# Kernel optimization log

Hardware: AMD Instinct MI355X
Metric: run time of the kernel (lower is better)

The kernel has to match this reference:

```python
import jax, jax.numpy as jnp
import numpy as np

N = 50000      # nodes
E = 800000     # edges
F = 128        # num_node_features
H = 128        # hidden_dim
DEPTH = 4
G = 512        # number of graphs in batch
BN_EPS = 1e-5


def setup_inputs() -> dict:
    key = jax.random.key(0)
    ks = jax.random.split(key, 10)
    x = jax.random.normal(ks[0], (N, F), dtype=jnp.float32)
    edge_index = jax.random.randint(ks[1], (2, E), 0, N, dtype=jnp.int64)
    batch = jnp.sort(jax.random.randint(ks[2], (N,), 0, G, dtype=jnp.int64))
    W_emb = jax.random.normal(ks[3], (F, H), dtype=jnp.float32) / np.sqrt(F)
    b_emb = jnp.zeros((H,), dtype=jnp.float32)
    W_conv = jax.random.normal(ks[4], (DEPTH, H, H), dtype=jnp.float32) / np.sqrt(H)
    b_conv = jnp.zeros((DEPTH, H), dtype=jnp.float32)
    gamma = jnp.ones((DEPTH - 1, H), dtype=jnp.float32)
    beta = jnp.zeros((DEPTH - 1, H), dtype=jnp.float32)
    return {"x": x, "edge_index": edge_index, "batch": batch,
            "W_emb": W_emb, "b_emb": b_emb, "W_conv": W_conv,
            "b_conv": b_conv, "gamma": gamma, "beta": beta}


def _gcn_conv(h, W, b, src, dst, dinv):
    # PyG GCNConv: D^{-1/2}(A+I)D^{-1/2} (h W) + b, with self-loops folded in
    hw = h @ W  # [N, H]
    norm = dinv[src] * dinv[dst]  # [E]
    agg = jax.ops.segment_sum(norm[:, None] * hw[src], dst, num_segments=N)
    agg = agg + (dinv * dinv)[:, None] * hw  # self-loop contribution
    return agg + b


def _batchnorm(h, g, b):
    mu = jnp.mean(h, axis=0)
    var = jnp.var(h, axis=0)
    return (h - mu) * jax.lax.rsqrt(var + BN_EPS) * g + b


def reference(x, edge_index, batch, W_emb, b_emb, W_conv, b_conv, gamma, beta):
    src, dst = edge_index[0], edge_index[1]
    # degrees incl. self-loop for symmetric GCN normalization
    deg = jax.ops.segment_sum(jnp.ones((E,), jnp.float32), dst, num_segments=N) + 1.0
    dinv = jax.lax.rsqrt(deg)
    h = x @ W_emb + b_emb  # embedding Linear
    for i in range(DEPTH):
        h = _gcn_conv(h, W_conv[i], b_conv[i], src, dst, dinv)
        if i < DEPTH - 1:
            h = jax.nn.relu(h)
            h = _batchnorm(h, gamma[i], beta[i])
    # global mean pool over graph ids
    counts = jax.ops.segment_sum(jnp.ones((N,), jnp.float32), batch, num_segments=G)
    pooled = jax.ops.segment_sum(h, batch, num_segments=G)
    return pooled / jnp.maximum(counts, 1.0)[:, None]
```

## Files before the change

kernel.cpp:

```cpp
#include <hip/hip_runtime.h>
#include <hip/hip_fp16.h>
#include <math.h>

#define HDIM 128
#define BKT_SHIFT 7
#define NBMAX 512
#define CHUNK 4096

typedef __attribute__((ext_vector_type(8))) short bf16x8;
typedef __attribute__((ext_vector_type(4))) float f32x4;

union U4 { unsigned int u[4]; bf16x8 v; };

__device__ __forceinline__ unsigned int cvt_pk_bf16(float a, float b) {
    unsigned int r;
    asm("v_cvt_pk_bf16_f32 %0, %1, %2" : "=v"(r) : "v"(a), "v"(b));
    return r;
}

__device__ __forceinline__ void split8(const float* v, bf16x8& ah, bf16x8& al) {
    U4 H, L;
    #pragma unroll
    for (int p = 0; p < 4; p++) {
        unsigned int h = cvt_pk_bf16(v[2 * p], v[2 * p + 1]);
        H.u[p] = h;
        float h0 = __uint_as_float(h << 16);
        float h1 = __uint_as_float(h & 0xFFFF0000u);
        L.u[p] = cvt_pk_bf16(v[2 * p] - h0, v[2 * p + 1] - h1);
    }
    ah = H.v; al = L.v;
}

__global__ __launch_bounds__(256) void bucket_hist(const int* __restrict__ dst,
                                                   int* __restrict__ bcount, int E) {
    __shared__ int h[NBMAX];
    int t = threadIdx.x;
    for (int b = t; b < NBMAX; b += 256) h[b] = 0;
    __syncthreads();
    int i = blockIdx.x * blockDim.x + t;
    int stride = gridDim.x * blockDim.x;
    for (; i < E; i += stride) atomicAdd(&h[dst[i] >> BKT_SHIFT], 1);
    __syncthreads();
    for (int b = t; b < NBMAX; b += 256) {
        int c = h[b];
        if (c) atomicAdd(&bcount[b], c);
    }
}

__global__ __launch_bounds__(256) void bucket_scan(const int* __restrict__ bcount,
                                                   int* __restrict__ bases,
                                                   int* __restrict__ cursor, int E) {
    int t = threadIdx.x;
    int v0 = bcount[2 * t], v1 = bcount[2 * t + 1];
    int s = v0 + v1;
    __shared__ int ss[256];
    ss[t] = s; __syncthreads();
    #pragma unroll
    for (int off = 1; off < 256; off <<= 1) {
        int u = (t >= off) ? ss[t - off] : 0;
        __syncthreads();
        ss[t] += u;
        __syncthreads();
    }
    int ex = ss[t] - s;
    bases[2 * t] = ex;          cursor[2 * t] = ex;
    bases[2 * t + 1] = ex + v0; cursor[2 * t + 1] = ex + v0;
    if (t == 255) bases[NBMAX] = E;
}

__global__ __launch_bounds__(256) void bucket_scatter(const int* __restrict__ src,
                                                      const int* __restrict__ dst,
                                                      int* __restrict__ cursor,
                                                      unsigned* __restrict__ ebuf, int E) {
    __shared__ unsigned sbuf[CHUNK];
    __shared__ int hist[NBMAX], hbase[NBMAX], gbase[NBMAX], cnt2[NBMAX];
    __shared__ int ss[256];
    int t = threadIdx.x;
    int start = blockIdx.x * CHUNK;
    int n = min(CHUNK, E - start);

    for (int b = t; b < NBMAX; b += 256) { hist[b] = 0; cnt2[b] = 0; }
    __syncthreads();
    for (int i = t; i < n; i += 256) atomicAdd(&hist[dst[start + i] >> BKT_SHIFT], 1);
    __syncthreads();

    int v0 = hist[2 * t], v1 = hist[2 * t + 1];
    int s = v0 + v1;
    ss[t] = s; __syncthreads();
    #pragma unroll
    for (int off = 1; off < 256; off <<= 1) {
        int u = (t >= off) ? ss[t - off] : 0;
        __syncthreads();
        ss[t] += u;
        __syncthreads();
    }
    int ex = ss[t] - s;
    hbase[2 * t] = ex;
    hbase[2 * t + 1] = ex + v0;
    if (v0 > 0) gbase[2 * t] = atomicAdd(&cursor[2 * t], v0);
    if (v1 > 0) gbase[2 * t + 1] = atomicAdd(&cursor[2 * t + 1], v1);
    __syncthreads();

    for (int i = t; i < n; i += 256) {
        int d = dst[start + i];
        int bkt = d >> BKT_SHIFT;
        unsigned p = ((unsigned)(d & 127) << 24) | (unsigned)src[start + i];
        int pos = atomicAdd(&cnt2[bkt], 1);
        sbuf[hbase[bkt] + pos] = p;
    }
    __syncthreads();

    for (int b = t; b < NBMAX; b += 256) {
        int c = hist[b], hb = hbase[b], gb = gbase[b];
        for (int j = 0; j < c; j++) ebuf[gb + j] = sbuf[hb + j];
    }
}

__global__ __launch_bounds__(256) void bucket_finalize(const unsigned* __restrict__ ebuf,
                                                       const int* __restrict__ bases,
                                                       int* __restrict__ csr,
                                                       int* __restrict__ offs,
                                                       float* __restrict__ dinv,
                                                       int N, int E) {
    int b = blockIdx.x;
    int beg = bases[b], end = bases[b + 1];
    __shared__ int hist[128], pre[128], cnt2[128];
    int t = threadIdx.x;
    if (t < 128) { hist[t] = 0; cnt2[t] = 0; }
    __syncthreads();
    for (int i = beg + t; i < end; i += 256)
        atomicAdd(&hist[(ebuf[i] >> 24) & 127], 1);
    __syncthreads();
    if (t < 128) pre[t] = hist[t];
    __syncthreads();
    #pragma unroll
    for (int off = 1; off < 128; off <<= 1) {
        int v = (t < 128 && t >= off) ? pre[t - off] : 0;
        __syncthreads();
        if (t < 128) pre[t] += v;
        __syncthreads();
    }
    if (t < 128) {
        int node = b * 128 + t;
        if (node < N) {
            int ex = pre[t] - hist[t];
            offs[node] = beg + ex;
            dinv[node] = rsqrtf((float)hist[t] + 1.0f);
        }
    }
    if (b == 0 && t == 0) offs[N] = E;
    __syncthreads();
    for (int i = beg + t; i < end; i += 256) {
        unsigned p = ebuf[i];
        int dl = (p >> 24) & 127;
        int pos = atomicAdd(&cnt2[dl], 1);
        csr[beg + (pre[dl] - hist[dl]) + pos] = (int)(p & 0xFFFFFFu);
    }
}

__global__ void wsplit_kernel(const float* __restrict__ Wsrc, short* __restrict__ Whi,
                              short* __restrict__ Wlo) {
    int i = blockIdx.x * 256 + threadIdx.x;
    if (i >= 128 * 128) return;
    int n = i >> 7, k = i & 127;
    float v = Wsrc[k * 128 + n];
    unsigned int u = __float_as_uint(v);
    unsigned int hi = (u + 0x7FFFu + ((u >> 16) & 1)) & 0xFFFF0000u;
    float hf = __uint_as_float(hi);
    float lo = v - hf;
    unsigned int ul = __float_as_uint(lo);
    unsigned int lo16 = (ul + 0x7FFFu + ((ul >> 16) & 1)) >> 16;
    Whi[i] = (short)(hi >> 16);
    Wlo[i] = (short)lo16;
}

template <bool OUT_F16>
__global__ __launch_bounds__(256) void gemm_mfma(const float* __restrict__ A,
                                                 const short* __restrict__ Wh,
                                                 const short* __restrict__ Wl,
                                                 const float* __restrict__ aff_s,
                                                 const float* __restrict__ aff_t,
                                                 const float* __restrict__ bias,
                                                 const float* __restrict__ rowscale,
                                                 void* __restrict__ outp, int N) {
    int w = threadIdx.x >> 6;
    int lane = threadIdx.x & 63;
    int l15 = lane & 15, lg = lane >> 4;
    int r0 = blockIdx.x * 128 + (w >> 1) * 64;
    int c0 = (w & 1) * 64;

    f32x4 acc[4][4];
    #pragma unroll
    for (int tc = 0; tc < 4; tc++) {
        float bz = bias ? bias[c0 + tc * 16 + l15] : 0.0f;
        #pragma unroll
        for (int tr = 0; tr < 4; tr++) {
            acc[tr][tc][0] = bz; acc[tr][tc][1] = bz;
            acc[tr][tc][2] = bz; acc[tr][tc][3] = bz;
        }
    }

    #pragma unroll
    for (int kt = 0; kt < 4; kt++) {
        int kk = kt * 32 + lg * 8;

        bf16x8 bh[4], bl[4];
        #pragma unroll
        for (int tc = 0; tc < 4; tc++) {
            int n = c0 + tc * 16 + l15;
            bh[tc] = *(const bf16x8*)(Wh + n * 128 + kk);
            bl[tc] = *(const bf16x8*)(Wl + n * 128 + kk);
        }

        float sv[8], tv[8];
        if (aff_s) {
            *(float4*)&sv[0] = *(const float4*)(aff_s + kk);
            *(float4*)&sv[4] = *(const float4*)(aff_s + kk + 4);
            *(float4*)&tv[0] = *(const float4*)(aff_t + kk);
            *(float4*)&tv[4] = *(const float4*)(aff_t + kk + 4);
        }

        bf16x8 ah[4], al[4];
        #pragma unroll
        for (int tr = 0; tr < 4; tr++) {
            int row = min(r0 + tr * 16 + l15, N - 1);
            const float* ap = A + (size_t)row * 128 + kk;
            float v[8];
            *(float4*)&v[0] = *(const float4*)ap;
            *(float4*)&v[4] = *(const float4*)(ap + 4);
            if (aff_s) {
                #pragma unroll
                for (int j = 0; j < 8; j++) v[j] = fmaf(v[j], sv[j], tv[j]);
            }
            split8(v, ah[tr], al[tr]);
        }

        #pragma unroll
        for (int tr = 0; tr < 4; tr++) {
            #pragma unroll
            for (int tc = 0; tc < 4; tc++) {
                acc[tr][tc] = __builtin_amdgcn_mfma_f32_16x16x32_bf16(ah[tr], bh[tc], acc[tr][tc], 0, 0, 0);
                acc[tr][tc] = __builtin_amdgcn_mfma_f32_16x16x32_bf16(ah[tr], bl[tc], acc[tr][tc], 0, 0, 0);
                acc[tr][tc] = __builtin_amdgcn_mfma_f32_16x16x32_bf16(al[tr], bh[tc], acc[tr][tc], 0, 0, 0);
            }
        }
    }

    #pragma unroll
    for (int tr = 0; tr < 4; tr++) {
        #pragma unroll
        for (int r = 0; r < 4; r++) {
            int row = r0 + tr * 16 + lg * 4 + r;
            if (row < N) {
                float sc = rowscale ? rowscale[row] : 1.0f;
                #pragma unroll
                for (int tc = 0; tc < 4; tc++) {
                    int col = c0 + tc * 16 + l15;
                    float val = acc[tr][tc][r] * sc;
                    if (OUT_F16) {
                        ((__half*)outp)[(size_t)row * 128 + col] = __float2half(val);
                    } else {
                        ((float*)outp)[(size_t)row * 128 + col] = val;
                    }
                }
            }
        }
    }
}

__global__ __launch_bounds__(256) void gather_kernel(const __half* __restrict__ hws,
                                                     const int* __restrict__ csr_src,
                                                     const int* __restrict__ offs,
                                                     const float* __restrict__ dinv,
                                                     const float* __restrict__ bias,
                                                     float* __restrict__ out,
                                                     int N, int relu) {
    int lane = threadIdx.x & 63;
    int node = blockIdx.x * 4 + (threadIdx.x >> 6);
    if (node >= N) return;
    int lo = offs[node], hi = offs[node + 1];

    float2 acc = make_float2(0.f, 0.f);
    int j = lo;
    for (; j + 3 < hi; j += 4) {
        int s0 = csr_src[j], s1 = csr_src[j + 1], s2 = csr_src[j + 2], s3 = csr_src[j + 3];
        float2 v0 = __half22float2(((const __half2*)(hws + (size_t)s0 * HDIM))[lane]);
        float2 v1 = __half22float2(((const __half2*)(hws + (size_t)s1 * HDIM))[lane]);
        float2 v2 = __half22float2(((const __half2*)(hws + (size_t)s2 * HDIM))[lane]);
        float2 v3 = __half22float2(((const __half2*)(hws + (size_t)s3 * HDIM))[lane]);
        acc.x += v0.x + v1.x + v2.x + v3.x;
        acc.y += v0.y + v1.y + v2.y + v3.y;
    }
    for (; j < hi; j++) {
        int s = csr_src[j];
        float2 v = __half22float2(((const __half2*)(hws + (size_t)s * HDIM))[lane]);
        acc.x += v.x; acc.y += v.y;
    }
    float2 vs = __half22float2(((const __half2*)(hws + (size_t)node * HDIM))[lane]);
    float di = dinv[node];
    float2 b = ((const float2*)bias)[lane];
    float ox = di * (acc.x + vs.x) + b.x;
    float oy = di * (acc.y + vs.y) + b.y;
    if (relu) { ox = fmaxf(ox, 0.f); oy = fmaxf(oy, 0.f); }
    ((float2*)(out + (size_t)node * HDIM))[lane] = make_float2(ox, oy);
}

__global__ __launch_bounds__(256) void bn_stats_kernel(const float* __restrict__ h,
                                                       float* __restrict__ stats, int N) {
    int f = threadIdx.x & 127;
    int half_ = threadIdx.x >> 7;
    float s = 0.f, s2 = 0.f;
    for (int n = blockIdx.x * 2 + half_; n < N; n += gridDim.x * 2) {
        float v = h[(size_t)n * HDIM + f];
        s += v;
        s2 += v * v;
    }
    __shared__ float ls[256], ls2[256];
    ls[threadIdx.x] = s;
    ls2[threadIdx.x] = s2;
    __syncthreads();
    if (half_ == 0) {
        s = ls[f] + ls[f + 128];
        s2 = ls2[f] + ls2[f + 128];
        atomicAdd(&stats[f], s);
        atomicAdd(&stats[128 + f], s2);
    }
}

__global__ void bn_finalize(const float* __restrict__ stats, const float* __restrict__ gamma,
                            const float* __restrict__ beta, float* __restrict__ aff_s,
                            float* __restrict__ aff_t, int N) {
    int f = threadIdx.x;
    float inv = 1.0f / (float)N;
    float m = stats[f] * inv;
    float var = stats[128 + f] * inv - m * m;
    float s = gamma[f] * rsqrtf(var + 1e-5f);
    aff_s[f] = s;
    aff_t[f] = beta[f] - m * s;
}

__device__ __forceinline__ int lower_bound_i(const int* __restrict__ arr, int n, int val) {
    int lo = 0, hi = n;
    while (lo < hi) {
        int mid = (lo + hi) >> 1;
        if (arr[mid] < val) lo = mid + 1; else hi = mid;
    }
    return lo;
}

__global__ void pool_kernel(const float* __restrict__ h, const int* __restrict__ batch,
                            float* __restrict__ out, int N, int G) {
    int g = blockIdx.x;
    int lo = lower_bound_i(batch, N, g);
    int hi = lower_bound_i(batch, N, g + 1);
    int f = threadIdx.x;
    float s = 0.f;
    for (int n = lo; n < hi; n++) s += h[(size_t)n * HDIM + f];
    float cnt = (float)(hi - lo);
    out[(size_t)g * HDIM + f] = s / fmaxf(cnt, 1.0f);
}

extern "C" void kernel_launch(void* const* d_in, const int* in_sizes, int n_in,
                              void* d_out, int out_size, void* d_ws, size_t ws_size,
                              hipStream_t stream) {
    const float* x      = (const float*)d_in[0];
    const int*   ei     = (const int*)d_in[1];
    const int*   batch  = (const int*)d_in[2];
    const float* W_emb  = (const float*)d_in[3];
    const float* b_emb  = (const float*)d_in[4];
    const float* W_conv = (const float*)d_in[5];
    const float* b_conv = (const float*)d_in[6];
    const float* gamma  = (const float*)d_in[7];
    const float* beta   = (const float*)d_in[8];

    const int E = in_sizes[1] / 2;
    const int N = in_sizes[2];
    const int G = out_size / HDIM;
    const int DEPTH = 4;

    const int* srcp = ei;
    const int* dstp = ei + E;
    float* out = (float*)d_out;

    size_t NH = (size_t)N * HDIM;
    size_t npad = ((size_t)N + 63) & ~(size_t)63;
    size_t epad = ((size_t)E + 63) & ~(size_t)63;
    int nb = (N + 127) / 128;

    float* ws = (float*)d_ws;
    float* dinv    = ws;
    int*   offs    = (int*)(dinv + npad);
    int*   bases   = offs + npad + 64;
    int*   cursor  = bases + 1024;
    int*   bcount  = cursor + NBMAX;
    int*   csr     = bcount + NBMAX;
    unsigned* ebuf = (unsigned*)(csr + epad);
    float* stats   = (float*)(ebuf + epad);
    float* aff_s   = stats + 256;
    float* aff_t   = aff_s + 128;
    short* wt      = (short*)(aff_t + 128);
    float* hbuf    = (float*)(wt + 5 * 2 * 16384);
    __half* hws16  = (__half*)(hbuf + NH);

    wsplit_kernel<<<64, 256, 0, stream>>>(W_emb, wt, wt + 16384);
    for (int l = 0; l < DEPTH; l++) {
        short* whi = wt + (size_t)(l + 1) * 32768;
        wsplit_kernel<<<64, 256, 0, stream>>>(W_conv + (size_t)l * 16384, whi, whi + 16384);
    }

    hipMemsetAsync(bcount, 0, NBMAX * sizeof(int), stream);
    bucket_hist<<<256, 256, 0, stream>>>(dstp, bcount, E);
    bucket_scan<<<1, 256, 0, stream>>>(bcount, bases, cursor, E);
    bucket_scatter<<<(E + CHUNK - 1) / CHUNK, 256, 0, stream>>>(srcp, dstp, cursor, ebuf, E);
    bucket_finalize<<<nb, 256, 0, stream>>>(ebuf, bases, csr, offs, dinv, N, E);

    int gemm_blocks = (N + 127) / 128;

    gemm_mfma<false><<<gemm_blocks, 256, 0, stream>>>(x, wt, wt + 16384, nullptr, nullptr,
                                                      b_emb, nullptr, hbuf, N);

    int gather_blocks = (N + 3) / 4;

    for (int l = 0; l < DEPTH; l++) {
        short* whi = wt + (size_t)(l + 1) * 32768;
        gemm_mfma<true><<<gemm_blocks, 256, 0, stream>>>(hbuf, whi, whi + 16384,
                                                         (l > 0) ? aff_s : nullptr,
                                                         (l > 0) ? aff_t : nullptr,
                                                         nullptr, dinv, hws16, N);
        gather_kernel<<<gather_blocks, 256, 0, stream>>>(hws16, csr, offs, dinv,
                                                         b_conv + (size_t)l * HDIM, hbuf,
                                                         N, (l < DEPTH - 1) ? 1 : 0);
        if (l < DEPTH - 1) {
            hipMemsetAsync(stats, 0, 256 * sizeof(float), stream);
            bn_stats_kernel<<<512, 256, 0, stream>>>(hbuf, stats, N);
            bn_finalize<<<1, 128, 0, stream>>>(stats, gamma + (size_t)l * HDIM,
                                               beta + (size_t)l * HDIM, aff_s, aff_t, N);
        }
    }

    pool_kernel<<<G, HDIM, 0, stream>>>(hbuf, batch, out, N, G);
}
```

Before: 448.8 us.

## Fuse batchnorm statistics into persistent gather kernel and merge weight splits

The gather kernel becomes a grid-stride persistent kernel with 512 blocks that accumulates per-feature sum and sum of squares while writing outputs. It emits per-block partials that bn_finalize reduces deterministically. This removes the separate bn_stats pass over the hidden buffer, the memset and the atomics. The five weight-split launches are also merged into one. The cost is fewer resident blocks for the latency-bound gather, which may reduce memory-level parallelism compared with the original 12.5k-block launch.

```diff
diff --git a/kernel.cpp b/kernel.cpp
--- a/kernel.cpp
+++ b/kernel.cpp
@@ -6,6 +6,7 @@
 #define BKT_SHIFT 7
 #define NBMAX 512
 #define CHUNK 4096
+#define GATHER_BLOCKS 512
 
 typedef __attribute__((ext_vector_type(8))) short bf16x8;
 typedef __attribute__((ext_vector_type(4))) float f32x4;
@@ -158,20 +159,24 @@
     }
 }
 
-__global__ void wsplit_kernel(const float* __restrict__ Wsrc, short* __restrict__ Whi,
-                              short* __restrict__ Wlo) {
-    int i = blockIdx.x * 256 + threadIdx.x;
-    if (i >= 128 * 128) return;
+__global__ void wsplit_all(const float* __restrict__ W_emb, const float* __restrict__ W_conv,
+                           short* __restrict__ wt) {
+    int gid = blockIdx.x * 256 + threadIdx.x;
+    if (gid >= 5 * 16384) return;
+    int m = gid >> 14;
+    int i = gid & 16383;
     int n = i >> 7, k = i & 127;
-    float v = Wsrc[k * 128 + n];
+    const float* src = (m == 0) ? W_emb : (W_conv + (size_t)(m - 1) * 16384);
+    float v = src[k * 128 + n];
     unsigned int u = __float_as_uint(v);
     unsigned int hi = (u + 0x7FFFu + ((u >> 16) & 1)) & 0xFFFF0000u;
     float hf = __uint_as_float(hi);
     float lo = v - hf;
     unsigned int ul = __float_as_uint(lo);
     unsigned int lo16 = (ul + 0x7FFFu + ((ul >> 16) & 1)) >> 16;
+    short* Whi = wt + (size_t)m * 32768;
     Whi[i] = (short)(hi >> 16);
-    Wlo[i] = (short)lo16;
+    Whi[16384 + i] = (short)lo16;
 }
 
 template <bool OUT_F16>
@@ -274,69 +279,82 @@
                                                      const float* __restrict__ dinv,
                                                      const float* __restrict__ bias,
                                                      float* __restrict__ out,
+                                                     float* __restrict__ Psum,
+                                                     float* __restrict__ Qsum,
                                                      int N, int relu) {
     int lane = threadIdx.x & 63;
-    int node = blockIdx.x * 4 + (threadIdx.x >> 6);
-    if (node >= N) return;
-    int lo = offs[node], hi = offs[node + 1];
-
-    float2 acc = make_float2(0.f, 0.f);
-    int j = lo;
-    for (; j + 3 < hi; j += 4) {
-        int s0 = csr_src[j], s1 = csr_src[j + 1], s2 = csr_src[j + 2], s3 = csr_src[j + 3];
-        float2 v0 = __half22float2(((const __half2*)(hws + (size_t)s0 * HDIM))[lane]);
-        float2 v1 = __half22float2(((const __half2*)(hws + (size_t)s1 * HDIM))[lane]);
-        float2 v2 = __half22float2(((const __half2*)(hws + (size_t)s2 * HDIM))[lane]);
-        float2 v3 = __half22float2(((const __half2*)(hws + (size_t)s3 * HDIM))[lane]);
-        acc.x += v0.x + v1.x + v2.x + v3.x;
-        acc.y += v0.y + v1.y + v2.y + v3.y;
-    }
-    for (; j < hi; j++) {
-        int s = csr_src[j];
-        float2 v = __half22float2(((const __half2*)(hws + (size_t)s * HDIM))[lane]);
-        acc.x += v.x; acc.y += v.y;
-    }
-    float2 vs = __half22float2(((const __half2*)(hws + (size_t)node * HDIM))[lane]);
-    float di = dinv[node];
+    int wv = threadIdx.x >> 6;
     float2 b = ((const float2*)bias)[lane];
-    float ox = di * (acc.x + vs.x) + b.x;
-    float oy = di * (acc.y + vs.y) + b.y;
-    if (relu) { ox = fmaxf(ox, 0.f); oy = fmaxf(oy, 0.f); }
-    ((float2*)(out + (size_t)node * HDIM))[lane] = make_float2(ox, oy);
-}
-
-__global__ __launch_bounds__(256) void bn_stats_kernel(const float* __restrict__ h,
-                                                       float* __restrict__ stats, int N) {
-    int f = threadIdx.x & 127;
-    int half_ = threadIdx.x >> 7;
-    float s = 0.f, s2 = 0.f;
-    for (int n = blockIdx.x * 2 + half_; n < N; n += gridDim.x * 2) {
-        float v = h[(size_t)n * HDIM + f];
-        s += v;
-        s2 += v * v;
-    }
-    __shared__ float ls[256], ls2[256];
-    ls[threadIdx.x] = s;
-    ls2[threadIdx.x] = s2;
-    __syncthreads();
-    if (half_ == 0) {
-        s = ls[f] + ls[f + 128];
-        s2 = ls2[f] + ls2[f + 128];
-        atomicAdd(&stats[f], s);
-        atomicAdd(&stats[128 + f], s2);
-    }
-}
-
-__global__ void bn_finalize(const float* __restrict__ stats, const float* __restrict__ gamma,
-                            const float* __restrict__ beta, float* __restrict__ aff_s,
-                            float* __restrict__ aff_t, int N) {
+    float sx = 0.f, sy = 0.f, qx = 0.f, qy = 0.f;
+    int ngroups = (N + 3) >> 2;
+
+    for (int g = blockIdx.x; g < ngroups; g += gridDim.x) {
+        int node = g * 4 + wv;
+        if (node >= N) continue;
+        int lo = offs[node], hi = offs[node + 1];
+
+        float2 acc = make_float2(0.f, 0.f);
+        int j = lo;
+        for (; j + 3 < hi; j += 4) {
+            int s0 = csr_src[j], s1 = csr_src[j + 1], s2 = csr_src[j + 2], s3 = csr_src[j + 3];
+            float2 v0 = __half22float2(((const __half2*)(hws + (size_t)s0 * HDIM))[lane]);
+            float2 v1 = __half22float2(((const __half2*)(hws + (size_t)s1 * HDIM))[lane]);
+            float2 v2 = __half22float2(((const __half2*)(hws + (size_t)s2 * HDIM))[lane]);
+            float2 v3 = __half22float2(((const __half2*)(hws + (size_t)s3 * HDIM))[lane]);
+            acc.x += v0.x + v1.x + v2.x + v3.x;
+            acc.y += v0.y + v1.y + v2.y + v3.y;
+        }
+        for (; j < hi; j++) {
+            int s = csr_src[j];
+            float2 v = __half22float2(((const __half2*)(hws + (size_t)s * HDIM))[lane]);
+            acc.x += v.x; acc.y += v.y;
+        }
+        float2 vs = __half22float2(((const __half2*)(hws + (size_t)node * HDIM))[lane]);
+        float di = dinv[node];
+        float ox = di * (acc.x + vs.x) + b.x;
+        float oy = di * (acc.y + vs.y) + b.y;
+        if (relu) { ox = fmaxf(ox, 0.f); oy = fmaxf(oy, 0.f); }
+        ((float2*)(out + (size_t)node * HDIM))[lane] = make_float2(ox, oy);
+        sx += ox; qx += ox * ox;
+        sy += oy; qy += oy * oy;
+    }
+
+    if (Psum) {
+        __shared__ float red[4][256];
+        red[0][threadIdx.x] = sx; red[1][threadIdx.x] = sy;
+        red[2][threadIdx.x] = qx; red[3][threadIdx.x] = qy;
+        __syncthreads();
+        if (threadIdx.x < 64) {
+            int l = threadIdx.x;
+            float S0 = red[0][l] + red[0][l + 64] + red[0][l + 128] + red[0][l + 192];
+            float S1 = red[1][l] + red[1][l + 64] + red[1][l + 128] + red[1][l + 192];
+            float Q0 = red[2][l] + red[2][l + 64] + red[2][l + 128] + red[2][l + 192];
+            float Q1 = red[3][l] + red[3][l + 64] + red[3][l + 128] + red[3][l + 192];
+            size_t base = (size_t)blockIdx.x * HDIM;
+            Psum[base + 2 * l] = S0; Psum[base + 2 * l + 1] = S1;
+            Qsum[base + 2 * l] = Q0; Qsum[base + 2 * l + 1] = Q1;
+        }
+    }
+}
+
+__global__ void bn_finalize(const float* __restrict__ Psum, const float* __restrict__ Qsum,
+                            const float* __restrict__ gamma, const float* __restrict__ beta,
+                            float* __restrict__ aff_s, float* __restrict__ aff_t,
+                            int N, int nblk) {
     int f = threadIdx.x;
+    float s = 0.f, q = 0.f;
+    for (int bb = 0; bb < nblk; bb += 4) {
+        s += Psum[(size_t)bb * HDIM + f] + Psum[(size_t)(bb + 1) * HDIM + f]
+           + Psum[(size_t)(bb + 2) * HDIM + f] + Psum[(size_t)(bb + 3) * HDIM + f];
+        q += Qsum[(size_t)bb * HDIM + f] + Qsum[(size_t)(bb + 1) * HDIM + f]
+           + Qsum[(size_t)(bb + 2) * HDIM + f] + Qsum[(size_t)(bb + 3) * HDIM + f];
+    }
     float inv = 1.0f / (float)N;
-    float m = stats[f] * inv;
-    float var = stats[128 + f] * inv - m * m;
-    float s = gamma[f] * rsqrtf(var + 1e-5f);
-    aff_s[f] = s;
-    aff_t[f] = beta[f] - m * s;
+    float m = s * inv;
+    float var = q * inv - m * m;
+    float sc = gamma[f] * rsqrtf(var + 1e-5f);
+    aff_s[f] = sc;
+    aff_t[f] = beta[f] - m * sc;
 }
 
 __device__ __forceinline__ int lower_bound_i(const int* __restrict__ arr, int n, int val) {
@@ -395,18 +413,15 @@
     int*   bcount  = cursor + NBMAX;
     int*   csr     = bcount + NBMAX;
     unsigned* ebuf = (unsigned*)(csr + epad);
-    float* stats   = (float*)(ebuf + epad);
-    float* aff_s   = stats + 256;
+    float* Psum    = (float*)(ebuf + epad);
+    float* Qsum    = Psum + GATHER_BLOCKS * HDIM;
+    float* aff_s   = Qsum + GATHER_BLOCKS * HDIM;
     float* aff_t   = aff_s + 128;
     short* wt      = (short*)(aff_t + 128);
     float* hbuf    = (float*)(wt + 5 * 2 * 16384);
     __half* hws16  = (__half*)(hbuf + NH);
 
-    wsplit_kernel<<<64, 256, 0, stream>>>(W_emb, wt, wt + 16384);
-    for (int l = 0; l < DEPTH; l++) {
-        short* whi = wt + (size_t)(l + 1) * 32768;
-        wsplit_kernel<<<64, 256, 0, stream>>>(W_conv + (size_t)l * 16384, whi, whi + 16384);
-    }
+    wsplit_all<<<(5 * 16384 + 255) / 256, 256, 0, stream>>>(W_emb, W_conv, wt);
 
     hipMemsetAsync(bcount, 0, NBMAX * sizeof(int), stream);
     bucket_hist<<<256, 256, 0, stream>>>(dstp, bcount, E);
@@ -418,8 +433,6 @@
 
     gemm_mfma<false><<<gemm_blocks, 256, 0, stream>>>(x, wt, wt + 16384, nullptr, nullptr,
                                                       b_emb, nullptr, hbuf, N);
-
-    int gather_blocks = (N + 3) / 4;
 
     for (int l = 0; l < DEPTH; l++) {
         short* whi = wt + (size_t)(l + 1) * 32768;
@@ -427,14 +440,16 @@
                                                          (l > 0) ? aff_s : nullptr,
                                                          (l > 0) ? aff_t : nullptr,
                                                          nullptr, dinv, hws16, N);
-        gather_kernel<<<gather_blocks, 256, 0, stream>>>(hws16, csr, offs, dinv,
+        bool need_bn = (l < DEPTH - 1);
+        gather_kernel<<<GATHER_BLOCKS, 256, 0, stream>>>(hws16, csr, offs, dinv,
                                                          b_conv + (size_t)l * HDIM, hbuf,
-                                                         N, (l < DEPTH - 1) ? 1 : 0);
-        if (l < DEPTH - 1) {
-            hipMemsetAsync(stats, 0, 256 * sizeof(float), stream);
-            bn_stats_kernel<<<512, 256, 0, stream>>>(hbuf, stats, N);
-            bn_finalize<<<1, 128, 0, stream>>>(stats, gamma + (size_t)l * HDIM,
-                                               beta + (size_t)l * HDIM, aff_s, aff_t, N);
+                                                         need_bn ? Psum : nullptr,
+                                                         need_bn ? Qsum : nullptr,
+                                                         N, need_bn ? 1 : 0);
+        if (need_bn) {
+            bn_finalize<<<1, 128, 0, stream>>>(Psum, Qsum, gamma + (size_t)l * HDIM,
+                                               beta + (size_t)l * HDIM, aff_s, aff_t,
+                                               N, GATHER_BLOCKS);
         }
     }
 
```

New measurement: 727.8 us. +62.2%, slower.
